# Kernel optimization log

Measured on AMD Instinct MI355X. Metric: run time of the kernel, lower is better.

Reference implementation:

```python
import jax, jax.numpy as jnp
import numpy as np

FLOAT_EPS = float(np.finfo(np.float32).eps)  # matches torch.finfo(torch.float32).eps


def setup_inputs() -> dict:
    key = jax.random.key(0)
    k0, k1, k2, k3, k4 = jax.random.split(key, 5)
    B, P, I, O, L = 16, 8192, 256, 128, 256  # batch, points, in_shapes, out_shapes, RNN_LATENT_SIZE
    x = jax.random.uniform(k0, (B, P, I), dtype=jnp.float32)
    latent_vector = jax.random.normal(k1, (B, L), dtype=jnp.float32)
    comp1 = 0.1 * jax.random.normal(k2, (L, I, O), dtype=jnp.float32)  # nn.init.normal_(std=0.1)
    comp2 = 0.1 * jax.random.normal(k3, (L, I, O), dtype=jnp.float32)
    temperature = jnp.full((1,), 2.0, dtype=jnp.float32)  # init.constant_(2)
    u = jax.random.uniform(k4, (B, 2, 1, I, O), dtype=jnp.float32)  # gumbel base noise (rand_like)
    return {"x": x, "latent_vector": latent_vector, "comp1": comp1,
            "comp2": comp2, "temperature": temperature, "u": u}


def reference(x, latent_vector, comp1, comp2, temperature, u):
    # mask_l/r: [B, I, O], softmax over the in-shapes axis (dim=-2)
    mask_l = jax.nn.softmax(jnp.einsum('bl,lio->bio', latent_vector, comp1), axis=-2)
    mask_r = jax.nn.softmax(jnp.einsum('bl,lio->bio', latent_vector, comp2), axis=-2)
    mask = jnp.stack([mask_l, mask_r], axis=1)[:, :, None]  # [B, 2, 1, I, O]

    # gumbel-softmax sampling: temperature clamp(eps, 2) then clamp_min(0.001)
    temp = jnp.maximum(jnp.clip(temperature, FLOAT_EPS, 2.0), 0.001)  # shape (1,)
    g = -jnp.log(-jnp.log(jnp.maximum(u, FLOAT_EPS)))
    mask_s = jax.nn.softmax((jnp.log(mask + FLOAT_EPS) + g) / temp, axis=-2)  # [B,2,1,I,O]

    # select: per-head broadcast-multiply-reduce == batched GEMM [B,P,I] x [B,2,I,O]
    sel = jnp.einsum('bpi,bkio->bpko', x, mask_s[:, :, 0])  # [B, P, 2, O]
    a, b = sel[:, :, 0], sel[:, :, 1]

    # arithmetic combine (union, intersection-ish, diffs) + clamp
    out = jnp.concatenate([a + b, a + b - 1.0, a - b, b - a], axis=-1)  # [B, P, 4*O]
    return jnp.clip(out, 0.0, 1.0)
```

## Files before the change

### kernel.cpp

```cpp
#include <hip/hip_runtime.h>
#include <hip/hip_bf16.h>

#define FLOAT_EPS 1.1920928955078125e-07f

typedef float f32x4 __attribute__((ext_vector_type(4)));
typedef short s16x8 __attribute__((ext_vector_type(8)));

#define B_ 16
#define P_ 8192
#define I_ 256
#define O_ 128
#define L_ 256
#define IO_ (I_*O_)

__device__ __forceinline__ float clip01(float v) {
    return fminf(fmaxf(v, 0.0f), 1.0f);
}
__device__ __forceinline__ f32x4 clip01v(f32x4 v) {
    f32x4 r;
    r[0] = clip01(v[0]); r[1] = clip01(v[1]);
    r[2] = clip01(v[2]); r[3] = clip01(v[3]);
    return r;
}

__global__ __launch_bounds__(256) void rl_k1_logits(
        const float* __restrict__ lat,
        const float* __restrict__ c1, const float* __restrict__ c2,
        float* __restrict__ lgP) {
    const int n  = blockIdx.x * 256 + threadIdx.x;
    const int ks = blockIdx.y;
    const int lh = blockIdx.z;
    const float* __restrict__ C  = (ks ? c2 : c1) + (size_t)lh * 128 * IO_;
    const int lbase = lh * 128;

    float acc[16];
#pragma unroll
    for (int b = 0; b < 16; ++b) acc[b] = 0.0f;

#pragma unroll 4
    for (int l = 0; l < 128; ++l) {
        float cv = C[(size_t)l * IO_ + n];
#pragma unroll
        for (int b = 0; b < 16; ++b)
            acc[b] += lat[b * L_ + lbase + l] * cv;
    }
    float* o = lgP + ((size_t)(lh * 32 + ks * 16)) * IO_ + n;
#pragma unroll
    for (int b = 0; b < 16; ++b) o[(size_t)b * IO_] = acc[b];
}

__global__ __launch_bounds__(256) void rl_k2_mask(
        const float* __restrict__ lgP, const float* __restrict__ u,
        const float* __restrict__ temp_p, __hip_bfloat16* __restrict__ MTF) {
    const int oo = threadIdx.x & 15;
    const int g  = threadIdx.x >> 4;
    const int o0 = blockIdx.x * 16;
    const int ks = blockIdx.y;
    const int b  = blockIdx.z;

    __shared__ float slab[I_][16];
    __shared__ float red[16][16];

    const float* __restrict__ z0 = lgP + (size_t)(ks * 16 + b) * IO_ + o0 + oo;
    const float* __restrict__ z1 = z0 + (size_t)32 * IO_;
    const float* __restrict__ up = u + ((size_t)b * 2 + ks) * IO_ + o0 + oo;

    float T = temp_p[0];
    T = fminf(fmaxf(T, FLOAT_EPS), 2.0f);
    T = fmaxf(T, 0.001f);
    const float rT = 1.0f / T;

    const int i0 = g * 16, i1 = i0 + 16;

    for (int i = i0; i < i1; ++i)
        slab[i][oo] = z0[(size_t)i * O_] + z1[(size_t)i * O_];
    __syncthreads();

    float m = -INFINITY;
    for (int i = i0; i < i1; ++i) m = fmaxf(m, slab[i][oo]);
    red[g][oo] = m; __syncthreads();
    m = -INFINITY;
#pragma unroll
    for (int j = 0; j < 16; ++j) m = fmaxf(m, red[j][oo]);
    __syncthreads();

    float S = 0.0f;
    for (int i = i0; i < i1; ++i) S += expf(slab[i][oo] - m);
    red[g][oo] = S; __syncthreads();
    S = 0.0f;
#pragma unroll
    for (int j = 0; j < 16; ++j) S += red[j][oo];
    __syncthreads();
    const float invS = 1.0f / S;

    float m2 = -INFINITY;
    for (int i = i0; i < i1; ++i) {
        float p  = expf(slab[i][oo] - m) * invS;
        float uu = fmaxf(up[(size_t)i * O_], FLOAT_EPS);
        float gg = -logf(-logf(uu));
        float s  = (logf(p + FLOAT_EPS) + gg) * rT;
        slab[i][oo] = s;
        m2 = fmaxf(m2, s);
    }
    red[g][oo] = m2; __syncthreads();
    m2 = -INFINITY;
#pragma unroll
    for (int j = 0; j < 16; ++j) m2 = fmaxf(m2, red[j][oo]);
    __syncthreads();

    float S2 = 0.0f;
    for (int i = i0; i < i1; ++i) S2 += expf(slab[i][oo] - m2);
    red[g][oo] = S2; __syncthreads();
    S2 = 0.0f;
#pragma unroll
    for (int j = 0; j < 16; ++j) S2 += red[j][oo];
    const float invS2 = 1.0f / S2;

    const int n  = ks * 128 + o0 + oo;
    const int f  = n >> 4;
    const int j0 = (f * 8 + (g >> 1)) * 64 + (g & 1) * 32 + oo;
    s16x8* __restrict__ MTFb = (s16x8*)MTF + (size_t)b * 8192;

    union { s16x8 v; __hip_bfloat162 h[4]; } c0, c1;
#pragma unroll
    for (int e = 0; e < 8; e += 2) {
        float v0 = expf(slab[i0 + e][oo]     - m2) * invS2;
        float v1 = expf(slab[i0 + e + 1][oo] - m2) * invS2;
        c0.h[e >> 1] = __float22bfloat162_rn(make_float2(v0, v1));
        float w0 = expf(slab[i0 + 8 + e][oo]     - m2) * invS2;
        float w1 = expf(slab[i0 + 8 + e + 1][oo] - m2) * invS2;
        c1.h[e >> 1] = __float22bfloat162_rn(make_float2(w0, w1));
    }
    MTFb[j0]      = c0.v;
    MTFb[j0 + 16] = c1.v;
}

__global__ __launch_bounds__(1024, 4) void rl_k3_gemm(
        const float* __restrict__ X, const __hip_bfloat16* __restrict__ MTF,
        float* __restrict__ OUT) {
    const int tid  = threadIdx.x;
    const int lane = tid & 63, wid = tid >> 6;
    const int b    = blockIdx.y;

    __shared__ s16x8 BF[8192];

    const float* __restrict__ Xb    = X + (size_t)b * P_ * I_;
    const s16x8* __restrict__ MTFb  = (const s16x8*)MTF + (size_t)b * 8192;
    float* __restrict__ Ob          = OUT + (size_t)b * P_ * 512;

    const int l15 = lane & 15, lhi = lane >> 4;
    const int rowbase = blockIdx.x * 512 + wid * 32 + l15;

    float4 raw[16];
    {
        const float* s0 = Xb + (size_t)rowbase * I_ + lhi * 8;
#pragma unroll
        for (int kk = 0; kk < 8; ++kk) {
            raw[2 * kk]     = *(const float4*)(s0 + kk * 32);
            raw[2 * kk + 1] = *(const float4*)(s0 + kk * 32 + 4);
        }
    }

#pragma unroll
    for (int it = 0; it < 8; ++it) {
        int j = it * 1024 + tid;
        BF[j] = MTFb[j];
    }
    __syncthreads();

    const float* s1 = Xb + (size_t)(rowbase + 16) * I_ + lhi * 8;

    {
        s16x8 af[8];
#pragma unroll
        for (int kk = 0; kk < 8; ++kk) {
            float4 f0 = raw[2 * kk], f1 = raw[2 * kk + 1];
            union { s16x8 v; __hip_bfloat162 h[4]; } cv;
            cv.h[0] = __float22bfloat162_rn(make_float2(f0.x, f0.y));
            cv.h[1] = __float22bfloat162_rn(make_float2(f0.z, f0.w));
            cv.h[2] = __float22bfloat162_rn(make_float2(f1.x, f1.y));
            cv.h[3] = __float22bfloat162_rn(make_float2(f1.z, f1.w));
            af[kk] = cv.v;
        }
        const int prow = blockIdx.x * 512 + wid * 32 + l15;
        float* __restrict__ oprow = Ob + (size_t)prow * 512 + lhi * 4;

#pragma unroll
        for (int fn = 0; fn < 8; ++fn) {
            raw[2 * fn]     = *(const float4*)(s1 + fn * 32);
            raw[2 * fn + 1] = *(const float4*)(s1 + fn * 32 + 4);
            __builtin_amdgcn_sched_barrier(0);

            f32x4 acc_a = (f32x4){0.f, 0.f, 0.f, 0.f};
            f32x4 acc_b = (f32x4){0.f, 0.f, 0.f, 0.f};
            const s16x8* pA = BF + (fn * 8) * 64 + lane;
            const s16x8* pB = BF + ((fn + 8) * 8) * 64 + lane;
#pragma unroll
            for (int kk = 0; kk < 8; ++kk) {
                s16x8 bfa = pA[kk * 64];
                s16x8 bfb = pB[kk * 64];
                acc_a = __builtin_amdgcn_mfma_f32_16x16x32_bf16(bfa, af[kk], acc_a, 0, 0, 0);
                acc_b = __builtin_amdgcn_mfma_f32_16x16x32_bf16(bfb, af[kk], acc_b, 0, 0, 0);
            }
            f32x4 s = acc_a + acc_b;
            float* op = oprow + fn * 16;
            __builtin_nontemporal_store(clip01v(s),             (f32x4*)(op));
            __builtin_nontemporal_store(clip01v(s - 1.0f),      (f32x4*)(op + 128));
            __builtin_nontemporal_store(clip01v(acc_a - acc_b), (f32x4*)(op + 256));
            __builtin_nontemporal_store(clip01v(acc_b - acc_a), (f32x4*)(op + 384));
            __builtin_amdgcn_sched_barrier(0);
        }
    }

    {
        s16x8 af[8];
#pragma unroll
        for (int kk = 0; kk < 8; ++kk) {
            float4 f0 = raw[2 * kk], f1 = raw[2 * kk + 1];
            union { s16x8 v; __hip_bfloat162 h[4]; } cv;
            cv.h[0] = __float22bfloat162_rn(make_float2(f0.x, f0.y));
            cv.h[1] = __float22bfloat162_rn(make_float2(f0.z, f0.w));
            cv.h[2] = __float22bfloat162_rn(make_float2(f1.x, f1.y));
            cv.h[3] = __float22bfloat162_rn(make_float2(f1.z, f1.w));
            af[kk] = cv.v;
        }
        const int prow = blockIdx.x * 512 + wid * 32 + 16 + l15;
        float* __restrict__ oprow = Ob + (size_t)prow * 512 + lhi * 4;

#pragma unroll
        for (int fn = 0; fn < 8; ++fn) {
            f32x4 acc_a = (f32x4){0.f, 0.f, 0.f, 0.f};
            f32x4 acc_b = (f32x4){0.f, 0.f, 0.f, 0.f};
            const s16x8* pA = BF + (fn * 8) * 64 + lane;
            const s16x8* pB = BF + ((fn + 8) * 8) * 64 + lane;
#pragma unroll
            for (int kk = 0; kk < 8; ++kk) {
                s16x8 bfa = pA[kk * 64];
                s16x8 bfb = pB[kk * 64];
                acc_a = __builtin_amdgcn_mfma_f32_16x16x32_bf16(bfa, af[kk], acc_a, 0, 0, 0);
                acc_b = __builtin_amdgcn_mfma_f32_16x16x32_bf16(bfb, af[kk], acc_b, 0, 0, 0);
            }
            f32x4 s = acc_a + acc_b;
            float* op = oprow + fn * 16;
            __builtin_nontemporal_store(clip01v(s),             (f32x4*)(op));
            __builtin_nontemporal_store(clip01v(s - 1.0f),      (f32x4*)(op + 128));
            __builtin_nontemporal_store(clip01v(acc_a - acc_b), (f32x4*)(op + 256));
            __builtin_nontemporal_store(clip01v(acc_b - acc_a), (f32x4*)(op + 384));
        }
    }
}

extern "C" void kernel_launch(void* const* d_in, const int* in_sizes, int n_in,
                              void* d_out, int out_size, void* d_ws, size_t ws_size,
                              hipStream_t stream) {
    const float* x    = (const float*)d_in[0];
    const float* lat  = (const float*)d_in[1];
    const float* c1   = (const float*)d_in[2];
    const float* c2   = (const float*)d_in[3];
    const float* temp = (const float*)d_in[4];
    const float* u    = (const float*)d_in[5];
    float* out = (float*)d_out;

    char* ws = (char*)d_ws;
    float*          lgP = (float*)ws;
    __hip_bfloat16* MTF = (__hip_bfloat16*)(ws + (8 << 20));

    rl_k1_logits<<<dim3(128, 2, 2), 256, 0, stream>>>(lat, c1, c2, lgP);
    rl_k2_mask  <<<dim3(8, 2, 16), 256, 0, stream>>>(lgP, u, temp, MTF);
    rl_k3_gemm  <<<dim3(16, 16), 1024, 0, stream>>>(x, MTF, out);
}
```

Baseline: 132.9 us.

## Split GEMM blocks across output-column halves and smaller row slabs

```diff
diff --git a/kernel.cpp b/kernel.cpp
--- a/kernel.cpp
+++ b/kernel.cpp
@@ -135,21 +135,23 @@
     MTFb[j0 + 16] = c1.v;
 }
 
-__global__ __launch_bounds__(1024, 4) void rl_k3_gemm(
+__global__ __launch_bounds__(512, 4) void rl_k3_gemm(
         const float* __restrict__ X, const __hip_bfloat16* __restrict__ MTF,
         float* __restrict__ OUT) {
     const int tid  = threadIdx.x;
     const int lane = tid & 63, wid = tid >> 6;
-    const int b    = blockIdx.y;
-
-    __shared__ s16x8 BF[8192];
+    const int zh   = blockIdx.x;
+    const int slab = blockIdx.y;
+    const int b    = blockIdx.z;
+
+    __shared__ s16x8 BF[4096];
 
     const float* __restrict__ Xb    = X + (size_t)b * P_ * I_;
     const s16x8* __restrict__ MTFb  = (const s16x8*)MTF + (size_t)b * 8192;
     float* __restrict__ Ob          = OUT + (size_t)b * P_ * 512;
 
     const int l15 = lane & 15, lhi = lane >> 4;
-    const int rowbase = blockIdx.x * 512 + wid * 32 + l15;
+    const int rowbase = slab * 256 + wid * 32 + l15;
 
     float4 raw[16];
     {
@@ -162,9 +164,10 @@
     }
 
 #pragma unroll
-    for (int it = 0; it < 8; ++it) {
-        int j = it * 1024 + tid;
-        BF[j] = MTFb[j];
+    for (int it = 0; it < 4; ++it) {
+        int j = it * 512 + tid;
+        BF[j]        = MTFb[zh * 2048 + j];
+        BF[2048 + j] = MTFb[4096 + zh * 2048 + j];
     }
     __syncthreads();
 
@@ -182,33 +185,33 @@
             cv.h[3] = __float22bfloat162_rn(make_float2(f1.z, f1.w));
             af[kk] = cv.v;
         }
-        const int prow = blockIdx.x * 512 + wid * 32 + l15;
+#pragma unroll
+        for (int kk = 0; kk < 8; ++kk) {
+            raw[2 * kk]     = *(const float4*)(s1 + kk * 32);
+            raw[2 * kk + 1] = *(const float4*)(s1 + kk * 32 + 4);
+        }
+        __builtin_amdgcn_sched_barrier(0);
+
+        const int prow = slab * 256 + wid * 32 + l15;
         float* __restrict__ oprow = Ob + (size_t)prow * 512 + lhi * 4;
 
 #pragma unroll
-        for (int fn = 0; fn < 8; ++fn) {
-            raw[2 * fn]     = *(const float4*)(s1 + fn * 32);
-            raw[2 * fn + 1] = *(const float4*)(s1 + fn * 32 + 4);
-            __builtin_amdgcn_sched_barrier(0);
-
+        for (int fl = 0; fl < 4; ++fl) {
             f32x4 acc_a = (f32x4){0.f, 0.f, 0.f, 0.f};
             f32x4 acc_b = (f32x4){0.f, 0.f, 0.f, 0.f};
-            const s16x8* pA = BF + (fn * 8) * 64 + lane;
-            const s16x8* pB = BF + ((fn + 8) * 8) * 64 + lane;
+            const s16x8* pA = BF + fl * 512 + lane;
+            const s16x8* pB = BF + 2048 + fl * 512 + lane;
 #pragma unroll
             for (int kk = 0; kk < 8; ++kk) {
-                s16x8 bfa = pA[kk * 64];
-                s16x8 bfb = pB[kk * 64];
-                acc_a = __builtin_amdgcn_mfma_f32_16x16x32_bf16(bfa, af[kk], acc_a, 0, 0, 0);
-                acc_b = __builtin_amdgcn_mfma_f32_16x16x32_bf16(bfb, af[kk], acc_b, 0, 0, 0);
+                acc_a = __builtin_amdgcn_mfma_f32_16x16x32_bf16(pA[kk * 64], af[kk], acc_a, 0, 0, 0);
+                acc_b = __builtin_amdgcn_mfma_f32_16x16x32_bf16(pB[kk * 64], af[kk], acc_b, 0, 0, 0);
             }
             f32x4 s = acc_a + acc_b;
-            float* op = oprow + fn * 16;
+            float* op = oprow + (zh * 4 + fl) * 16;
             __builtin_nontemporal_store(clip01v(s),             (f32x4*)(op));
             __builtin_nontemporal_store(clip01v(s - 1.0f),      (f32x4*)(op + 128));
             __builtin_nontemporal_store(clip01v(acc_a - acc_b), (f32x4*)(op + 256));
             __builtin_nontemporal_store(clip01v(acc_b - acc_a), (f32x4*)(op + 384));
-            __builtin_amdgcn_sched_barrier(0);
         }
     }
 
@@ -224,24 +227,22 @@
             cv.h[3] = __float22bfloat162_rn(make_float2(f1.z, f1.w));
             af[kk] = cv.v;
         }
-        const int prow = blockIdx.x * 512 + wid * 32 + 16 + l15;
+        const int prow = slab * 256 + wid * 32 + 16 + l15;
         float* __restrict__ oprow = Ob + (size_t)prow * 512 + lhi * 4;
 
 #pragma unroll
-        for (int fn = 0; fn < 8; ++fn) {
+        for (int fl = 0; fl < 4; ++fl) {
             f32x4 acc_a = (f32x4){0.f, 0.f, 0.f, 0.f};
             f32x4 acc_b = (f32x4){0.f, 0.f, 0.f, 0.f};
-            const s16x8* pA = BF + (fn * 8) * 64 + lane;
-            const s16x8* pB = BF + ((fn + 8) * 8) * 64 + lane;
+            const s16x8* pA = BF + fl * 512 + lane;
+            const s16x8* pB = BF + 2048 + fl * 512 + lane;
 #pragma unroll
             for (int kk = 0; kk < 8; ++kk) {
-                s16x8 bfa = pA[kk * 64];
-                s16x8 bfb = pB[kk * 64];
-                acc_a = __builtin_amdgcn_mfma_f32_16x16x32_bf16(bfa, af[kk], acc_a, 0, 0, 0);
-                acc_b = __builtin_amdgcn_mfma_f32_16x16x32_bf16(bfb, af[kk], acc_b, 0, 0, 0);
+                acc_a = __builtin_amdgcn_mfma_f32_16x16x32_bf16(pA[kk * 64], af[kk], acc_a, 0, 0, 0);
+                acc_b = __builtin_amdgcn_mfma_f32_16x16x32_bf16(pB[kk * 64], af[kk], acc_b, 0, 0, 0);
             }
             f32x4 s = acc_a + acc_b;
-            float* op = oprow + fn * 16;
+            float* op = oprow + (zh * 4 + fl) * 16;
             __builtin_nontemporal_store(clip01v(s),             (f32x4*)(op));
             __builtin_nontemporal_store(clip01v(s - 1.0f),      (f32x4*)(op + 128));
             __builtin_nontemporal_store(clip01v(acc_a - acc_b), (f32x4*)(op + 256));
@@ -267,5 +268,5 @@
 
     rl_k1_logits<<<dim3(128, 2, 2), 256, 0, stream>>>(lat, c1, c2, lgP);
     rl_k2_mask  <<<dim3(8, 2, 16), 256, 0, stream>>>(lgP, u, temp, MTF);
-    rl_k3_gemm  <<<dim3(16, 16), 1024, 0, stream>>>(x, MTF, out);
-}
+    rl_k3_gemm  <<<dim3(2, 32, 16), 512, 0, stream>>>(x, MTF, out);
+}
```

Result: slower. 136.7 us (+2.8%).
